# Performance work log

Hardware: AMD Instinct MI355X
Metric: run time of the kernel (lower is better)

The kernel has to match this reference:

```python
import jax, jax.numpy as jnp
import numpy as np

B = 256
H = W = 14
HW = H * W
TS = 0.03  # sigmoid temperature
TC = 0.07  # contrastive temperature
TP_K = int(HW * 0.1)   # 19
TN_K = int(HW * 0.5)   # 98
EPS_NORM = 1e-12
EPS_PD = 1e-6  # torch F.pairwise_distance eps


def _l2norm(x, axis):
    n = jnp.sqrt(jnp.sum(x * x, axis=axis, keepdims=True))
    return x / jnp.maximum(n, EPS_NORM)


def _conv(x, w):
    return jax.lax.conv_general_dilated(
        x, w, window_strides=(1, 1), padding='SAME',
        dimension_numbers=('NCHW', 'OIHW', 'NCHW'))


def setup_inputs() -> dict:
    key = jax.random.key(0)
    ks = jax.random.split(key, 7)
    ev = jax.random.normal(ks[0], (B, 384, H, W), dtype=jnp.float32)
    ea = jax.random.normal(ks[1], (B, 2048), dtype=jnp.float32)
    masks = jax.random.randint(ks[2], (B, H, W), 0, 2).astype(jnp.int32)
    masks = masks.at[:, 0, 0].set(1)  # guarantee nonzero mask area
    W_fc1 = jax.random.normal(ks[3], (512, 2048), dtype=jnp.float32) * 0.02
    W_fc2 = jax.random.normal(ks[4], (512, 512), dtype=jnp.float32) * 0.02
    W_conv1 = jax.random.normal(ks[5], (512, 384, 3, 3), dtype=jnp.float32) * 0.02
    W_conv2 = jax.random.normal(ks[6], (512, 512, 3, 3), dtype=jnp.float32) * 0.02
    return {'ev': ev, 'ea': ea, 'masks': masks, 'W_fc1': W_fc1,
            'W_fc2': W_fc2, 'W_conv1': W_conv1, 'W_conv2': W_conv2}


def reference(ev, ea, masks, W_fc1, W_fc2, W_conv1, W_conv2):
    # Audio_Proj: fc2(relu(fc1(ea)))  -> (B, 512)
    fa = jnp.maximum(ea @ W_fc1.T, 0.0) @ W_fc2.T

    # Visual_Proj: conv2(relu(conv1(ev))) -> (B, 512, 14, 14)
    fv_map = _conv(jnp.maximum(_conv(ev, W_conv1), 0.0), W_conv2)
    fv_map_norm = _l2norm(fv_map, axis=1)

    # masked mean pooling over the Ncut mask -> indicator vector (B, 512)
    m = masks.astype(jnp.float32)
    ind_vec = jnp.sum(fv_map * m[:, None], axis=(2, 3)) / jnp.sum(m, axis=(1, 2))[:, None]
    ind_vec_norm = _l2norm(ind_vec, axis=1)

    # Sij[i, j, p] = <fv_map_norm[i, :, p], ind_vec_norm[j]>  -> (B, B, HW)
    Sij = jnp.einsum('ichw,jc->ijhw', fv_map_norm, ind_vec_norm).reshape(B, B, HW)

    # per-row topk thresholds (kth largest / kth smallest)
    pos_thr = jax.lax.top_k(Sij, TP_K)[0][..., -1:]           # (B, B, 1)
    neg_thr = -jax.lax.top_k(-Sij, TN_K)[0][..., -1:]         # (B, B, 1)

    m_p = jax.nn.sigmoid((Sij - pos_thr) / TS)
    m_n = 1.0 - jax.nn.sigmoid((Sij - neg_thr) / TS)

    SP = jnp.sum(Sij * m_p, axis=-1) / jnp.sum(m_p, axis=-1)  # (B, B)
    SN = jnp.sum(Sij * m_n, axis=-1) / jnp.sum(m_n, axis=-1)  # (B, B)

    logits1 = jnp.concatenate([SP, SN], axis=1) / TC          # (B, 2B)
    logits2 = jnp.concatenate([SP.T, SN.T], axis=1) / TC
    labels = jnp.arange(B)
    loss1 = -jnp.mean(jax.nn.log_softmax(logits1, axis=-1)[labels, labels])
    loss2 = -jnp.mean(jax.nn.log_softmax(logits2, axis=-1)[labels, labels])

    # squared pairwise distance between detached ind_vec and fa (torch eps in diff)
    diff = jax.lax.stop_gradient(ind_vec)[:, None, :] - fa[None, :, :] + EPS_PD
    dist_mat = jnp.sum(diff * diff, axis=-1)                  # (B, B)

    ivn_d = jax.lax.stop_gradient(ind_vec_norm)
    vv_logits = ivn_d @ ivn_d.T
    eye = jnp.eye(B, dtype=jnp.float32)
    w = -vv_logits * (1.0 - eye) + eye
    dist_mat = dist_mat * w

    mask_mat = eye - (1.0 - eye) / (B - 1)
    loss3 = jnp.mean(jnp.maximum(jnp.sum(dist_mat * mask_mat, axis=1) + 0.6, 0.0))
    loss4 = jnp.mean(jnp.maximum(jnp.sum(dist_mat * mask_mat, axis=0) + 0.6, 0.0))

    return ((loss1 + loss2) / 2.0, (loss3 + loss4) / 2.0)
```

## Files before the change

kernel.cpp:

```cpp
#include <hip/hip_runtime.h>
#include <stdint.h>


typedef __attribute__((ext_vector_type(8))) short bf16x8;
typedef __attribute__((ext_vector_type(4))) float f32x4;

__device__ __forceinline__ unsigned short f2bf(float x) {
  unsigned u = __float_as_uint(x);
  unsigned r = u + 0x7FFFu + ((u >> 16) & 1u);
  return (unsigned short)(r >> 16);
}
__device__ __forceinline__ float bf2f(unsigned short h) {
  return __uint_as_float(((unsigned)h) << 16);
}

typedef const __attribute__((address_space(1))) void* gptr1_t;
typedef __attribute__((address_space(3))) void* lptr3_t;
__device__ __forceinline__ void gload_lds16(const void* g, void* l) {
  __builtin_amdgcn_global_load_lds((gptr1_t)g, (lptr3_t)l, 16, 0, 0);
}

__device__ __forceinline__ float waveSum(float v) {
#pragma unroll
  for (int m = 1; m < 64; m <<= 1) v += __shfl_xor(v, m, 64);
  return v;
}
__device__ __forceinline__ float waveMax(float v) {
#pragma unroll
  for (int m = 1; m < 64; m <<= 1) v = fmaxf(v, __shfl_xor(v, m, 64));
  return v;
}
template <int NW>
__device__ __forceinline__ float blockSum(float v) {
  __shared__ float sh[NW];
  v = waveSum(v);
  int wv = threadIdx.x >> 6, ln = threadIdx.x & 63;
  if (ln == 0) sh[wv] = v;
  __syncthreads();
  float r = 0.f;
#pragma unroll
  for (int w = 0; w < NW; ++w) r += sh[w];
  __syncthreads();
  return r;
}
template <int NW>
__device__ __forceinline__ float blockMax(float v) {
  __shared__ float sh[NW];
  v = waveMax(v);
  int wv = threadIdx.x >> 6, ln = threadIdx.x & 63;
  if (ln == 0) sh[wv] = v;
  __syncthreads();
  float r = -3.4e38f;
#pragma unroll
  for (int w = 0; w < NW; ++w) r = fmaxf(r, sh[w]);
  __syncthreads();
  return r;
}

template <int K, int NT, int NTOT, int NLD, bool APAD, bool OPAD, int EPI>
__global__ __launch_bounds__(256, 2) void gemm_k(
    const unsigned short* __restrict__ A, const unsigned short* __restrict__ Bw,
    void* __restrict__ C) {
  __shared__ short As[128 * 64];
  __shared__ short Bs[128 * 64];
  const int tid = threadIdx.x;
  const int wave = tid >> 6, lane = tid & 63;
  const int m0 = blockIdx.x * 128, n0 = blockIdx.y * 128;
  const int rr8 = lane >> 3;
  const int seg = lane & 7;
  const int gseg = seg ^ rr8;
  const int wm = wave >> 1, wn = wave & 1;
  const int quad = lane >> 4, tq = lane & 15;

  int asrc[4], bsrc[4];
#pragma unroll
  for (int i8 = 0; i8 < 4; ++i8) {
    int rloc = wave * 32 + i8 * 8 + rr8;
    int m = m0 + rloc;
    int sr;
    if (APAD) {
      int b = m / 196, p = m - b * 196, h = p / 14, w = p - h * 14;
      sr = b * 256 + (h + 1) * 16 + (w + 1);
    } else
      sr = m;
    asrc[i8] = sr * K + gseg * 8;
    bsrc[i8] = (n0 + rloc) * K + gseg * 8;
  }

  short* As_st[4];
  short* Bs_st[4];
#pragma unroll
  for (int i8 = 0; i8 < 4; ++i8) {
    As_st[i8] = &As[(wave * 32 + i8 * 8) * 64];
    Bs_st[i8] = &Bs[(wave * 32 + i8 * 8) * 64];
  }

  f32x4 acc[4][4];
#pragma unroll
  for (int mi = 0; mi < 4; ++mi)
#pragma unroll
    for (int ni = 0; ni < 4; ++ni) {
      f32x4 z = {0.f, 0.f, 0.f, 0.f};
      acc[mi][ni] = z;
    }

#pragma unroll 1
  for (int t = 0; t < NT; ++t) {
    int adel = 0;
    if (NT > 1) {
      int dh = t / 3 - 1, dw = t - (t / 3) * 3 - 1;
      adel = (dh * 16 + dw) * K;
    }
    const unsigned short* Bt = Bw + (size_t)t * NTOT * K;
#pragma unroll 1
    for (int kc2 = 0; kc2 < K / 64; ++kc2) {
      int kb = kc2 * 64;
      __syncthreads();
#pragma unroll
      for (int i8 = 0; i8 < 4; ++i8)
        gload_lds16(A + asrc[i8] + adel + kb, As_st[i8]);
#pragma unroll
      for (int i8 = 0; i8 < 4; ++i8)
        gload_lds16(Bt + bsrc[i8] + kb, Bs_st[i8]);
      __syncthreads();
#pragma unroll
      for (int h = 0; h < 2; ++h) {
        bf16x8 af[4], bfr[4];
#pragma unroll
        for (int mi = 0; mi < 4; ++mi) {
          int row = wm * 64 + mi * 16 + tq;
          af[mi] = *(const bf16x8*)&As[row * 64 +
                                       (((h << 2) | quad) ^ (row & 7)) * 8];
        }
#pragma unroll
        for (int ni = 0; ni < 4; ++ni) {
          int row = wn * 64 + ni * 16 + tq;
          bfr[ni] = *(const bf16x8*)&Bs[row * 64 +
                                        (((h << 2) | quad) ^ (row & 7)) * 8];
        }
#pragma unroll
        for (int mi = 0; mi < 4; ++mi)
#pragma unroll
          for (int ni = 0; ni < 4; ++ni)
            acc[mi][ni] = __builtin_amdgcn_mfma_f32_16x16x32_bf16(
                af[mi], bfr[ni], acc[mi][ni], 0, 0, 0);
      }
    }
  }

#pragma unroll
  for (int mi = 0; mi < 4; ++mi) {
#pragma unroll
    for (int r = 0; r < 4; ++r) {
      int m = m0 + wm * 64 + mi * 16 + quad * 4 + r;
      int orow;
      if (OPAD) {
        int b = m / 196, p = m - b * 196, h = p / 14, w = p - h * 14;
        orow = b * 256 + (h + 1) * 16 + (w + 1);
      } else
        orow = m;
      size_t obase = (size_t)orow * NLD + n0 + wn * 64 + tq;
#pragma unroll
      for (int ni = 0; ni < 4; ++ni) {
        float v = acc[mi][ni][r];
        size_t idx = obase + ni * 16;
        if (EPI == 0)
          ((unsigned short*)C)[idx] = f2bf(fmaxf(v, 0.f));
        else if (EPI == 1)
          ((unsigned short*)C)[idx] = f2bf(v);
        else
          ((float*)C)[idx] = v;
      }
    }
  }
}


__global__ void prep_cast_k(const float* __restrict__ ea,
                            const float* __restrict__ Wf1,
                            const float* __restrict__ Wf2,
                            unsigned short* __restrict__ eab,
                            unsigned short* __restrict__ wf1b,
                            unsigned short* __restrict__ wf2b) {
  int i = blockIdx.x * 256 + threadIdx.x;
  if (i < 524288)
    eab[i] = f2bf(ea[i]);
  else if (i < 1572864)
    wf1b[i - 524288] = f2bf(Wf1[i - 524288]);
  else
    wf2b[i - 1572864] = f2bf(Wf2[i - 1572864]);
}

template <int CIN>
__global__ void build_wb_k(const float* __restrict__ W,
                           unsigned short* __restrict__ out) {
  int i = blockIdx.x * 256 + threadIdx.x;
  if (i >= 9 * 512 * CIN) return;
  int t = i / (512 * CIN);
  int rem = i - t * (512 * CIN);
  int n = rem / CIN;
  int c = rem - n * CIN;
  out[i] = f2bf(W[(n * CIN + c) * 9 + t]);
}

__global__ void evpad_k(const float* __restrict__ ev,
                        unsigned short* __restrict__ out) {
  int i = blockIdx.x * 256 + threadIdx.x;
  int pr = i / 384, c = i - pr * 384;
  int b = pr >> 8, cell = pr & 255;
  int h = (cell >> 4) - 1, w = (cell & 15) - 1;
  float v = 0.f;
  if ((unsigned)h < 14u && (unsigned)w < 14u)
    v = ev[(b * 384 + c) * 196 + h * 14 + w];
  out[i] = f2bf(v);
}

__global__ void halo_k(unsigned int* __restrict__ x1u) {
  int r = blockIdx.x;
  int b = r / 60, c = r - b * 60;
  int cell;
  if (c < 16) cell = c;
  else if (c < 32) cell = 240 + (c - 16);
  else if (c < 46) cell = (c - 31) * 16;
  else cell = (c - 45) * 16 + 15;
  x1u[(size_t)(b * 256 + cell) * 256 + threadIdx.x] = 0u;
}


__global__ __launch_bounds__(512) void pool_k(
    const unsigned short* __restrict__ fv, const int* __restrict__ masks,
    float* __restrict__ indv) {
  int b = blockIdx.x;
  int w = threadIdx.x >> 6, lane = threadIdx.x & 63;
  __shared__ float red[8][512];
  __shared__ float msh[8];
  float acc[8] = {0.f, 0.f, 0.f, 0.f, 0.f, 0.f, 0.f, 0.f};
  float msum = 0.f;
  for (int p = w; p < 196; p += 8) {
    float m = (float)masks[b * 196 + p];
    msum += m;
    uint4 d = *(const uint4*)(fv + (size_t)(b * 196 + p) * 512 + lane * 8);
    const unsigned short* hp = (const unsigned short*)&d;
#pragma unroll
    for (int k = 0; k < 8; ++k) acc[k] += m * bf2f(hp[k]);
  }
#pragma unroll
  for (int k = 0; k < 8; ++k) red[w][lane * 8 + k] = acc[k];
  if (lane == 0) msh[w] = msum;
  __syncthreads();
  int tid = threadIdx.x;
  float s = 0.f, mtot = 0.f;
#pragma unroll
  for (int ww = 0; ww < 8; ++ww) {
    s += red[ww][tid];
    mtot += msh[ww];
  }
  indv[b * 512 + tid] = s / mtot;
}

__global__ __launch_bounds__(512) void indnorm_k(
    const float* __restrict__ indv, float* __restrict__ indn,
    unsigned short* __restrict__ indnb, unsigned short* __restrict__ ivpb,
    float* __restrict__ Pi) {
  int b = blockIdx.x, tid = threadIdx.x;
  float v = indv[b * 512 + tid];
  float ss = blockSum<8>(v * v);
  float sc = 1.f / fmaxf(sqrtf(ss), 1e-12f);
  float o = v * sc;
  indn[b * 512 + tid] = o;
  indnb[b * 512 + tid] = f2bf(o);
  float ve = v + 1e-6f;
  ivpb[b * 512 + tid] = f2bf(ve);
  float p2 = blockSum<8>(ve * ve);
  if (tid == 0) Pi[b] = p2;
}

__global__ __launch_bounds__(512) void fanorm_k(const float* __restrict__ fa,
                                                unsigned short* __restrict__ fab,
                                                float* __restrict__ Qj) {
  int b = blockIdx.x, tid = threadIdx.x;
  float v = fa[b * 512 + tid];
  fab[b * 512 + tid] = f2bf(v);
  float q = blockSum<8>(v * v);
  if (tid == 0) Qj[b] = q;
}

__global__ __launch_bounds__(256) void rownorm_k(
    const unsigned short* __restrict__ fv, float* __restrict__ rn) {
  int row = blockIdx.x * 4 + (threadIdx.x >> 6);
  int lane = threadIdx.x & 63;
  uint4 d = *(const uint4*)(fv + (size_t)row * 512 + lane * 8);
  const unsigned short* hp = (const unsigned short*)&d;
  float ss = 0.f;
#pragma unroll
  for (int k = 0; k < 8; ++k) {
    float x = bf2f(hp[k]);
    ss += x * x;
  }
  ss = waveSum(ss);
  if (lane == 0) rn[row] = 1.f / fmaxf(sqrtf(ss), 1e-12f);
}


__device__ __forceinline__ float radix_kth(unsigned k0, unsigned k1, unsigned k2,
                                           unsigned k3, int k) {
  unsigned prefix = 0;
  int kk = k;
#pragma unroll 1
  for (int bit = 31; bit >= 8; --bit) {
    unsigned thi = (prefix >> bit) | 1u;
    int c = __popcll(__ballot((k0 >> bit) == thi)) +
            __popcll(__ballot((k1 >> bit) == thi)) +
            __popcll(__ballot((k2 >> bit) == thi)) +
            __popcll(__ballot((k3 >> bit) == thi));
    if (kk <= c)
      prefix |= (1u << bit);
    else
      kk -= c;
  }
  unsigned u = (prefix & 0x80000000u) ? (prefix ^ 0x80000000u) : ~prefix;
  return __uint_as_float(u);
}
__device__ __forceinline__ unsigned sortkey(float x) {
  unsigned u = __float_as_uint(x);
  return u ^ (((int)u >> 31) | 0x80000000u);
}

__global__ __launch_bounds__(256) void spsn_k(const float* __restrict__ Sij,
                                              const float* __restrict__ rn,
                                              float* __restrict__ SP,
                                              float* __restrict__ SN) {
  int i = blockIdx.x, jg = blockIdx.y;
  int tid = threadIdx.x, wave = tid >> 6, lane = tid & 63;
  __shared__ float tile[196 * 65];
#pragma unroll 1
  for (int it = 0; it < 49; ++it) {
    int lin = it * 256 + tid;
    int p = lin >> 6, j = lin & 63;
    tile[p * 65 + j] =
        Sij[(size_t)(i * 196 + p) * 256 + jg * 64 + j] * rn[i * 196 + p];
  }
  __syncthreads();
#pragma unroll 1
  for (int jj = 0; jj < 16; ++jj) {
    int j = jj * 4 + wave;
    float v0 = tile[lane * 65 + j];
    float v1 = tile[(lane + 64) * 65 + j];
    float v2 = tile[(lane + 128) * 65 + j];
    bool val3 = lane < 4;
    float v3 = val3 ? tile[(lane + 192) * 65 + j] : 0.f;
    unsigned k0 = sortkey(v0), k1 = sortkey(v1), k2 = sortkey(v2);
    unsigned k3 = val3 ? sortkey(v3) : 0u;
    float thrP = radix_kth(k0, k1, k2, k3, 19);
    float thrN = radix_kth(k0, k1, k2, k3, 99);
    float spn = 0.f, spd = 0.f, snn = 0.f, snd = 0.f;
    const float invTS = 1.f / 0.03f;
#pragma unroll
    for (int q = 0; q < 4; ++q) {
      float v = (q == 0) ? v0 : (q == 1) ? v1 : (q == 2) ? v2 : v3;
      bool ok = (q < 3) || val3;
      if (ok) {
        float mp = 1.f / (1.f + __expf((thrP - v) * invTS));
        float mn = 1.f / (1.f + __expf((v - thrN) * invTS));
        spn += v * mp;
        spd += mp;
        snn += v * mn;
        snd += mn;
      }
    }
    spn = waveSum(spn); spd = waveSum(spd);
    snn = waveSum(snn); snd = waveSum(snd);
    if (lane == 0) {
      SP[i * 256 + jg * 64 + j] = spn / spd;
      SN[i * 256 + jg * 64 + j] = snn / snd;
    }
  }
}

__global__ __launch_bounds__(256) void loss12_k(const float* __restrict__ SP,
                                                const float* __restrict__ SN,
                                                float* __restrict__ out) {
  int r = blockIdx.x;
  int i = r & 255;
  bool col = r >= 256;
  int tid = threadIdx.x;
  const float invTC = 1.f / 0.07f;
  float a = (col ? SP[tid * 256 + i] : SP[i * 256 + tid]) * invTC;
  float b = (col ? SN[tid * 256 + i] : SN[i * 256 + tid]) * invTC;
  float mx = blockMax<4>(fmaxf(a, b));
  float se = blockSum<4>(__expf(a - mx) + __expf(b - mx));
  float lse = mx + __logf(se);
  if (tid == 0) {
    float diag = SP[i * 256 + i] * invTC;
    atomicAdd(out, -(diag - lse) * (1.f / 512.f));
  }
}

__global__ __launch_bounds__(256) void distcomb_k(
    const float* __restrict__ Pi, const float* __restrict__ Qj,
    const float* __restrict__ X, const float* __restrict__ V,
    float* __restrict__ val, float* __restrict__ out) {
  int i = blockIdx.x, j = threadIdx.x;
  float d = Pi[i] - 2.f * X[i * 256 + j] + Qj[j];
  float w = (i == j) ? 1.f : -V[i * 256 + j];
  float x = d * w;
  val[i * 256 + j] = x;
  __shared__ float diag_sh;
  if (j == i) diag_sh = x;
  float tot = blockSum<4>(x);
  if (j == 0) {
    float rs = diag_sh - (tot - diag_sh) * (1.f / 255.f);
    atomicAdd(out + 1, fmaxf(rs + 0.6f, 0.f) * (1.f / 512.f));
  }
}

__global__ __launch_bounds__(256) void loss4_k(const float* __restrict__ val,
                                               float* __restrict__ out) {
  int j = blockIdx.x, i = threadIdx.x;
  float x = val[i * 256 + j];
  __shared__ float diag_sh;
  if (i == j) diag_sh = x;
  float tot = blockSum<4>(x);
  if (i == 0) {
    float cs = diag_sh - (tot - diag_sh) * (1.f / 255.f);
    atomicAdd(out + 1, fmaxf(cs + 0.6f, 0.f) * (1.f / 512.f));
  }
}


extern "C" void kernel_launch(void* const* d_in, const int* in_sizes, int n_in,
                              void* d_out, int out_size, void* d_ws,
                              size_t ws_size, hipStream_t stream) {
  (void)in_sizes; (void)n_in; (void)out_size; (void)ws_size;
  const float* ev = (const float*)d_in[0];
  const float* ea = (const float*)d_in[1];
  const int* msk = (const int*)d_in[2];
  const float* Wf1 = (const float*)d_in[3];
  const float* Wf2 = (const float*)d_in[4];
  const float* Wc1 = (const float*)d_in[5];
  const float* Wc2 = (const float*)d_in[6];
  float* out = (float*)d_out;
  char* ws = (char*)d_ws;

  size_t off = 0;
  auto alloc = [&](size_t bytes) {
    void* p = ws + off;
    off = (off + bytes + 255) & ~(size_t)255;
    return p;
  };
  unsigned short* evb = (unsigned short*)alloc(51380224);
  unsigned short* fv = evb;
  unsigned short* x1b = (unsigned short*)alloc((size_t)65536 * 512 * 2);
  float* Sij = (float*)x1b;
  unsigned short* wb1 = (unsigned short*)alloc((size_t)9 * 512 * 384 * 2);
  unsigned short* wb2 = (unsigned short*)alloc((size_t)9 * 512 * 512 * 2);
  unsigned short* eab = (unsigned short*)alloc((size_t)256 * 2048 * 2);
  unsigned short* wf1b = (unsigned short*)alloc((size_t)512 * 2048 * 2);
  unsigned short* wf2b = (unsigned short*)alloc((size_t)512 * 512 * 2);
  unsigned short* hb = (unsigned short*)alloc((size_t)256 * 512 * 2);
  float* fa = (float*)alloc((size_t)256 * 512 * 4);
  float* indv = (float*)alloc((size_t)256 * 512 * 4);
  float* indn = (float*)alloc((size_t)256 * 512 * 4);
  unsigned short* indnb = (unsigned short*)alloc((size_t)256 * 512 * 2);
  unsigned short* ivpb = (unsigned short*)alloc((size_t)256 * 512 * 2);
  unsigned short* fab = (unsigned short*)alloc((size_t)256 * 512 * 2);
  float* Pi = (float*)alloc(256 * 4);
  float* Qj = (float*)alloc(256 * 4);
  float* Xm = (float*)alloc((size_t)256 * 256 * 4);
  float* Vm = (float*)alloc((size_t)256 * 256 * 4);
  float* rn = (float*)alloc((size_t)50176 * 4);
  float* SP = (float*)alloc((size_t)256 * 256 * 4);
  float* SN = (float*)alloc((size_t)256 * 256 * 4);
  float* val = (float*)alloc((size_t)256 * 256 * 4);

  hipMemsetAsync(out, 0, 2 * sizeof(float), stream);

  prep_cast_k<<<7168, 256, 0, stream>>>(ea, Wf1, Wf2, eab, wf1b, wf2b);
  build_wb_k<384><<<(9 * 512 * 384) / 256, 256, 0, stream>>>(Wc1, wb1);
  build_wb_k<512><<<(9 * 512 * 512) / 256, 256, 0, stream>>>(Wc2, wb2);
  evpad_k<<<(65536 * 384) / 256, 256, 0, stream>>>(ev, evb);
  halo_k<<<15360, 256, 0, stream>>>((unsigned int*)x1b);

  gemm_k<384, 9, 512, 512, true, true, 0>
      <<<dim3(392, 4), 256, 0, stream>>>(evb, wb1, x1b);
  gemm_k<2048, 1, 512, 512, false, false, 0>
      <<<dim3(2, 4), 256, 0, stream>>>(eab, wf1b, hb);
  gemm_k<512, 1, 512, 512, false, false, 2>
      <<<dim3(2, 4), 256, 0, stream>>>(hb, wf2b, fa);
  gemm_k<512, 9, 512, 512, true, false, 1>
      <<<dim3(392, 4), 256, 0, stream>>>(x1b, wb2, fv);

  pool_k<<<256, 512, 0, stream>>>(fv, msk, indv);
  fanorm_k<<<256, 512, 0, stream>>>(fa, fab, Qj);
  indnorm_k<<<256, 512, 0, stream>>>(indv, indn, indnb, ivpb, Pi);
  rownorm_k<<<12544, 256, 0, stream>>>(fv, rn);

  gemm_k<512, 1, 256, 256, false, false, 2>
      <<<dim3(392, 2), 256, 0, stream>>>(fv, indnb, Sij);
  gemm_k<512, 1, 256, 256, false, false, 2>
      <<<dim3(2, 2), 256, 0, stream>>>(ivpb, fab, Xm);
  gemm_k<512, 1, 256, 256, false, false, 2>
      <<<dim3(2, 2), 256, 0, stream>>>(indnb, indnb, Vm);

  spsn_k<<<dim3(256, 4), 256, 0, stream>>>(Sij, rn, SP, SN);
  loss12_k<<<512, 256, 0, stream>>>(SP, SN, out);
  distcomb_k<<<256, 256, 0, stream>>>(Pi, Qj, Xm, Vm, val, out);
  loss4_k<<<256, 256, 0, stream>>>(val, out);
}
```

Baseline: 923.9 us.

## Reuse haloed activation tile across all nine conv taps with double-buffered weights

Replaces the per-tap implicit-GEMM conv loop with a kernel that loads a 256-row haloed window of padded activations once per K-chunk and reuses it for all nine taps, indexing shifted rows in LDS. Weight tiles for the next tap are prefetched into a second LDS buffer while the current tap computes. Activation global/L2 traffic per conv drops by about nine times, at the cost of more LDS and more barriers per chunk. Also coalesces the ev padding transpose through shared memory and folds the row-norm computation into the pooling kernel, removing a separate pass over fv.

After: 972.1 us. 1.05x slower.

```diff
diff --git a/kernel.cpp b/kernel.cpp
--- a/kernel.cpp
+++ b/kernel.cpp
@@ -57,8 +57,120 @@
   return r;
 }
 
-template <int K, int NT, int NTOT, int NLD, bool APAD, bool OPAD, int EPI>
-__global__ __launch_bounds__(256, 2) void gemm_k(
+__device__ __forceinline__ int padrow(int m) {
+  int b = m / 196, p = m - b * 196, h = p / 14, w = p - h * 14;
+  return b * 256 + (h + 1) * 16 + (w + 1);
+}
+
+template <int K, int EPI>
+__global__ __launch_bounds__(512, 4) void convtap_k(
+    const unsigned short* __restrict__ A, const unsigned short* __restrict__ Bw,
+    unsigned short* __restrict__ C) {
+  __shared__ short Ah[256 * 64];
+  __shared__ short Bb[2][128 * 64];
+  const int tid = threadIdx.x;
+  const int wave = tid >> 6, lane = tid & 63;
+  const int wm = wave >> 2, wn = wave & 3;
+  const int quad = lane >> 4, tq = lane & 15;
+  const int rr8 = lane >> 3, seg = lane & 7, gseg = seg ^ rr8;
+  const int m0 = blockIdx.x * 128, n0 = blockIdx.y * 128;
+  const int base = padrow(m0) - 17;
+
+  int prow[4];
+#pragma unroll
+  for (int mi = 0; mi < 4; ++mi)
+    prow[mi] = padrow(m0 + wm * 64 + mi * 16 + tq) - base;
+
+  size_t asrc[4];
+#pragma unroll
+  for (int i = 0; i < 4; ++i) {
+    int r = base + i * 64 + wave * 8 + rr8;
+    if (r > 65535) r = 65535;
+    asrc[i] = (size_t)r * K + gseg * 8;
+  }
+  size_t bsrc[2];
+#pragma unroll
+  for (int i = 0; i < 2; ++i)
+    bsrc[i] = (size_t)(n0 + i * 64 + wave * 8 + rr8) * K + gseg * 8;
+  const size_t btap = (size_t)512 * K;
+
+  f32x4 acc[4][2];
+#pragma unroll
+  for (int mi = 0; mi < 4; ++mi)
+#pragma unroll
+    for (int ni = 0; ni < 2; ++ni) {
+      f32x4 z = {0.f, 0.f, 0.f, 0.f};
+      acc[mi][ni] = z;
+    }
+
+#pragma unroll 1
+  for (int kc = 0; kc < K / 64; ++kc) {
+    const int kb = kc * 64;
+    __syncthreads();
+#pragma unroll
+    for (int i = 0; i < 4; ++i)
+      gload_lds16(A + asrc[i] + kb, &Ah[(i * 64 + wave * 8) * 64]);
+#pragma unroll
+    for (int i = 0; i < 2; ++i)
+      gload_lds16(Bw + bsrc[i] + kb, &Bb[0][(i * 64 + wave * 8) * 64]);
+    __syncthreads();
+#pragma unroll 1
+    for (int t = 0; t < 9; ++t) {
+      if (t < 8) {
+        const unsigned short* Bt1 = Bw + (size_t)(t + 1) * btap;
+#pragma unroll
+        for (int i = 0; i < 2; ++i)
+          gload_lds16(Bt1 + bsrc[i] + kb,
+                      &Bb[(t + 1) & 1][(i * 64 + wave * 8) * 64]);
+      }
+      int t3 = t / 3;
+      int delta = (t3 - 1) * 16 + (t - t3 * 3 - 1);
+      const short* Bcur = Bb[t & 1];
+#pragma unroll
+      for (int h = 0; h < 2; ++h) {
+        bf16x8 af[4], bfr[2];
+#pragma unroll
+        for (int mi = 0; mi < 4; ++mi) {
+          int r = prow[mi] + delta;
+          af[mi] = *(const bf16x8*)&Ah[r * 64 +
+                                       ((((h << 2) | quad) ^ (r & 7)) << 3)];
+        }
+#pragma unroll
+        for (int ni = 0; ni < 2; ++ni) {
+          int r = wn * 32 + ni * 16 + tq;
+          bfr[ni] = *(const bf16x8*)&Bcur[r * 64 +
+                                          ((((h << 2) | quad) ^ (r & 7)) << 3)];
+        }
+#pragma unroll
+        for (int mi = 0; mi < 4; ++mi)
+#pragma unroll
+          for (int ni = 0; ni < 2; ++ni)
+            acc[mi][ni] = __builtin_amdgcn_mfma_f32_16x16x32_bf16(
+                af[mi], bfr[ni], acc[mi][ni], 0, 0, 0);
+      }
+      if (t < 8) __syncthreads();
+    }
+  }
+
+#pragma unroll
+  for (int mi = 0; mi < 4; ++mi) {
+#pragma unroll
+    for (int r = 0; r < 4; ++r) {
+      int m = m0 + wm * 64 + mi * 16 + quad * 4 + r;
+      int orow = (EPI == 0) ? padrow(m) : m;
+      size_t ob = (size_t)orow * 512 + n0 + wn * 32 + tq;
+#pragma unroll
+      for (int ni = 0; ni < 2; ++ni) {
+        float v = acc[mi][ni][r];
+        if (EPI == 0) v = fmaxf(v, 0.f);
+        C[ob + ni * 16] = f2bf(v);
+      }
+    }
+  }
+}
+
+template <int K, int NLD, int EPI>
+__global__ __launch_bounds__(256, 2) void gemm1_k(
     const unsigned short* __restrict__ A, const unsigned short* __restrict__ Bw,
     void* __restrict__ C) {
   __shared__ short As[128 * 64];
@@ -66,33 +178,16 @@
   const int tid = threadIdx.x;
   const int wave = tid >> 6, lane = tid & 63;
   const int m0 = blockIdx.x * 128, n0 = blockIdx.y * 128;
-  const int rr8 = lane >> 3;
-  const int seg = lane & 7;
-  const int gseg = seg ^ rr8;
+  const int rr8 = lane >> 3, seg = lane & 7, gseg = seg ^ rr8;
   const int wm = wave >> 1, wn = wave & 1;
   const int quad = lane >> 4, tq = lane & 15;
 
-  int asrc[4], bsrc[4];
+  size_t asrc[4], bsrc[4];
 #pragma unroll
   for (int i8 = 0; i8 < 4; ++i8) {
     int rloc = wave * 32 + i8 * 8 + rr8;
-    int m = m0 + rloc;
-    int sr;
-    if (APAD) {
-      int b = m / 196, p = m - b * 196, h = p / 14, w = p - h * 14;
-      sr = b * 256 + (h + 1) * 16 + (w + 1);
-    } else
-      sr = m;
-    asrc[i8] = sr * K + gseg * 8;
-    bsrc[i8] = (n0 + rloc) * K + gseg * 8;
-  }
-
-  short* As_st[4];
-  short* Bs_st[4];
-#pragma unroll
-  for (int i8 = 0; i8 < 4; ++i8) {
-    As_st[i8] = &As[(wave * 32 + i8 * 8) * 64];
-    Bs_st[i8] = &Bs[(wave * 32 + i8 * 8) * 64];
+    asrc[i8] = (size_t)(m0 + rloc) * K + gseg * 8;
+    bsrc[i8] = (size_t)(n0 + rloc) * K + gseg * 8;
   }
 
   f32x4 acc[4][4];
@@ -105,46 +200,36 @@
     }
 
 #pragma unroll 1
-  for (int t = 0; t < NT; ++t) {
-    int adel = 0;
-    if (NT > 1) {
-      int dh = t / 3 - 1, dw = t - (t / 3) * 3 - 1;
-      adel = (dh * 16 + dw) * K;
-    }
-    const unsigned short* Bt = Bw + (size_t)t * NTOT * K;
-#pragma unroll 1
-    for (int kc2 = 0; kc2 < K / 64; ++kc2) {
-      int kb = kc2 * 64;
-      __syncthreads();
-#pragma unroll
-      for (int i8 = 0; i8 < 4; ++i8)
-        gload_lds16(A + asrc[i8] + adel + kb, As_st[i8]);
-#pragma unroll
-      for (int i8 = 0; i8 < 4; ++i8)
-        gload_lds16(Bt + bsrc[i8] + kb, Bs_st[i8]);
-      __syncthreads();
-#pragma unroll
-      for (int h = 0; h < 2; ++h) {
-        bf16x8 af[4], bfr[4];
-#pragma unroll
-        for (int mi = 0; mi < 4; ++mi) {
-          int row = wm * 64 + mi * 16 + tq;
-          af[mi] = *(const bf16x8*)&As[row * 64 +
-                                       (((h << 2) | quad) ^ (row & 7)) * 8];
-        }
-#pragma unroll
-        for (int ni = 0; ni < 4; ++ni) {
-          int row = wn * 64 + ni * 16 + tq;
-          bfr[ni] = *(const bf16x8*)&Bs[row * 64 +
-                                        (((h << 2) | quad) ^ (row & 7)) * 8];
-        }
-#pragma unroll
-        for (int mi = 0; mi < 4; ++mi)
-#pragma unroll
-          for (int ni = 0; ni < 4; ++ni)
-            acc[mi][ni] = __builtin_amdgcn_mfma_f32_16x16x32_bf16(
-                af[mi], bfr[ni], acc[mi][ni], 0, 0, 0);
-      }
+  for (int kc2 = 0; kc2 < K / 64; ++kc2) {
+    int kb = kc2 * 64;
+    __syncthreads();
+#pragma unroll
+    for (int i8 = 0; i8 < 4; ++i8) {
+      gload_lds16(A + asrc[i8] + kb, &As[(wave * 32 + i8 * 8) * 64]);
+      gload_lds16(Bw + bsrc[i8] + kb, &Bs[(wave * 32 + i8 * 8) * 64]);
+    }
+    __syncthreads();
+#pragma unroll
+    for (int h = 0; h < 2; ++h) {
+      bf16x8 af[4], bfr[4];
+#pragma unroll
+      for (int mi = 0; mi < 4; ++mi) {
+        int row = wm * 64 + mi * 16 + tq;
+        af[mi] = *(const bf16x8*)&As[row * 64 +
+                                     ((((h << 2) | quad) ^ (row & 7)) << 3)];
+      }
+#pragma unroll
+      for (int ni = 0; ni < 4; ++ni) {
+        int row = wn * 64 + ni * 16 + tq;
+        bfr[ni] = *(const bf16x8*)&Bs[row * 64 +
+                                      ((((h << 2) | quad) ^ (row & 7)) << 3)];
+      }
+#pragma unroll
+      for (int mi = 0; mi < 4; ++mi)
+#pragma unroll
+        for (int ni = 0; ni < 4; ++ni)
+          acc[mi][ni] = __builtin_amdgcn_mfma_f32_16x16x32_bf16(
+              af[mi], bfr[ni], acc[mi][ni], 0, 0, 0);
     }
   }
 
@@ -153,21 +238,13 @@
 #pragma unroll
     for (int r = 0; r < 4; ++r) {
       int m = m0 + wm * 64 + mi * 16 + quad * 4 + r;
-      int orow;
-      if (OPAD) {
-        int b = m / 196, p = m - b * 196, h = p / 14, w = p - h * 14;
-        orow = b * 256 + (h + 1) * 16 + (w + 1);
-      } else
-        orow = m;
-      size_t obase = (size_t)orow * NLD + n0 + wn * 64 + tq;
+      size_t obase = (size_t)m * NLD + n0 + wn * 64 + tq;
 #pragma unroll
       for (int ni = 0; ni < 4; ++ni) {
         float v = acc[mi][ni][r];
         size_t idx = obase + ni * 16;
         if (EPI == 0)
           ((unsigned short*)C)[idx] = f2bf(fmaxf(v, 0.f));
-        else if (EPI == 1)
-          ((unsigned short*)C)[idx] = f2bf(v);
         else
           ((float*)C)[idx] = v;
       }
@@ -203,16 +280,29 @@
   out[i] = f2bf(W[(n * CIN + c) * 9 + t]);
 }
 
-__global__ void evpad_k(const float* __restrict__ ev,
-                        unsigned short* __restrict__ out) {
-  int i = blockIdx.x * 256 + threadIdx.x;
-  int pr = i / 384, c = i - pr * 384;
-  int b = pr >> 8, cell = pr & 255;
-  int h = (cell >> 4) - 1, w = (cell & 15) - 1;
-  float v = 0.f;
-  if ((unsigned)h < 14u && (unsigned)w < 14u)
-    v = ev[(b * 384 + c) * 196 + h * 14 + w];
-  out[i] = f2bf(v);
+__global__ __launch_bounds__(256) void evpad_k(const float* __restrict__ ev,
+                                               unsigned short* __restrict__ out) {
+  int b = blockIdx.x, ct = blockIdx.y;
+  __shared__ float tile[64][197];
+  int tid = threadIdx.x;
+  const float* src = ev + ((size_t)b * 384 + ct * 64) * 196;
+#pragma unroll 1
+  for (int it = 0; it < 49; ++it) {
+    int idx = it * 256 + tid;
+    int c = idx / 196, p = idx - c * 196;
+    tile[c][p] = src[idx];
+  }
+  __syncthreads();
+  unsigned short* dst = out + (size_t)b * 256 * 384 + ct * 64;
+#pragma unroll 1
+  for (int it = 0; it < 64; ++it) {
+    int idx = it * 256 + tid;
+    int cell = idx >> 6, c = idx & 63;
+    int h = (cell >> 4) - 1, w = (cell & 15) - 1;
+    float v = ((unsigned)h < 14u && (unsigned)w < 14u) ? tile[c][h * 14 + w]
+                                                       : 0.f;
+    dst[(size_t)cell * 384 + c] = f2bf(v);
+  }
 }
 
 __global__ void halo_k(unsigned int* __restrict__ x1u) {
@@ -229,7 +319,7 @@
 
 __global__ __launch_bounds__(512) void pool_k(
     const unsigned short* __restrict__ fv, const int* __restrict__ masks,
-    float* __restrict__ indv) {
+    float* __restrict__ indv, float* __restrict__ rn) {
   int b = blockIdx.x;
   int w = threadIdx.x >> 6, lane = threadIdx.x & 63;
   __shared__ float red[8][512];
@@ -241,8 +331,15 @@
     msum += m;
     uint4 d = *(const uint4*)(fv + (size_t)(b * 196 + p) * 512 + lane * 8);
     const unsigned short* hp = (const unsigned short*)&d;
-#pragma unroll
-    for (int k = 0; k < 8; ++k) acc[k] += m * bf2f(hp[k]);
+    float ss = 0.f;
+#pragma unroll
+    for (int k = 0; k < 8; ++k) {
+      float x = bf2f(hp[k]);
+      ss += x * x;
+      acc[k] += m * x;
+    }
+    ss = waveSum(ss);
+    if (lane == 0) rn[b * 196 + p] = 1.f / fmaxf(sqrtf(ss), 1e-12f);
   }
 #pragma unroll
   for (int k = 0; k < 8; ++k) red[w][lane * 8 + k] = acc[k];
@@ -283,22 +380,6 @@
   fab[b * 512 + tid] = f2bf(v);
   float q = blockSum<8>(v * v);
   if (tid == 0) Qj[b] = q;
-}
-
-__global__ __launch_bounds__(256) void rownorm_k(
-    const unsigned short* __restrict__ fv, float* __restrict__ rn) {
-  int row = blockIdx.x * 4 + (threadIdx.x >> 6);
-  int lane = threadIdx.x & 63;
-  uint4 d = *(const uint4*)(fv + (size_t)row * 512 + lane * 8);
-  const unsigned short* hp = (const unsigned short*)&d;
-  float ss = 0.f;
-#pragma unroll
-  for (int k = 0; k < 8; ++k) {
-    float x = bf2f(hp[k]);
-    ss += x * x;
-  }
-  ss = waveSum(ss);
-  if (lane == 0) rn[row] = 1.f / fmaxf(sqrtf(ss), 1e-12f);
 }
 
 
@@ -448,7 +529,7 @@
     off = (off + bytes + 255) & ~(size_t)255;
     return p;
   };
-  unsigned short* evb = (unsigned short*)alloc(51380224);
+  unsigned short* evb = (unsigned short*)alloc((size_t)50176 * 512 * 2);
   unsigned short* fv = evb;
   unsigned short* x1b = (unsigned short*)alloc((size_t)65536 * 512 * 2);
   float* Sij = (float*)x1b;
@@ -478,29 +559,21 @@
   prep_cast_k<<<7168, 256, 0, stream>>>(ea, Wf1, Wf2, eab, wf1b, wf2b);
   build_wb_k<384><<<(9 * 512 * 384) / 256, 256, 0, stream>>>(Wc1, wb1);
   build_wb_k<512><<<(9 * 512 * 512) / 256, 256, 0, stream>>>(Wc2, wb2);
-  evpad_k<<<(65536 * 384) / 256, 256, 0, stream>>>(ev, evb);
+  evpad_k<<<dim3(256, 6), 256, 0, stream>>>(ev, evb);
   halo_k<<<15360, 256, 0, stream>>>((unsigned int*)x1b);
 
-  gemm_k<384, 9, 512, 512, true, true, 0>
-      <<<dim3(392, 4), 256, 0, stream>>>(evb, wb1, x1b);
-  gemm_k<2048, 1, 512, 512, false, false, 0>
-      <<<dim3(2, 4), 256, 0, stream>>>(eab, wf1b, hb);
-  gemm_k<512, 1, 512, 512, false, false, 2>
-      <<<dim3(2, 4), 256, 0, stream>>>(hb, wf2b, fa);
-  gemm_k<512, 9, 512, 512, true, false, 1>
-      <<<dim3(392, 4), 256, 0, stream>>>(x1b, wb2, fv);
-
-  pool_k<<<256, 512, 0, stream>>>(fv, msk, indv);
+  convtap_k<384, 0><<<dim3(392, 4), 512, 0, stream>>>(evb, wb1, x1b);
+  gemm1_k<2048, 512, 0><<<dim3(2, 4), 256, 0, stream>>>(eab, wf1b, hb);
+  gemm1_k<512, 512, 2><<<dim3(2, 4), 256, 0, stream>>>(hb, wf2b, fa);
+  convtap_k<512, 1><<<dim3(392, 4), 512, 0, stream>>>(x1b, wb2, fv);
+
+  pool_k<<<256, 512, 0, stream>>>(fv, msk, indv, rn);
   fanorm_k<<<256, 512, 0, stream>>>(fa, fab, Qj);
   indnorm_k<<<256, 512, 0, stream>>>(indv, indn, indnb, ivpb, Pi);
-  rownorm_k<<<12544, 256, 0, stream>>>(fv, rn);
-
-  gemm_k<512, 1, 256, 256, false, false, 2>
-      <<<dim3(392, 2), 256, 0, stream>>>(fv, indnb, Sij);
-  gemm_k<512, 1, 256, 256, false, false, 2>
-      <<<dim3(2, 2), 256, 0, stream>>>(ivpb, fab, Xm);
-  gemm_k<512, 1, 256, 256, false, false, 2>
-      <<<dim3(2, 2), 256, 0, stream>>>(indnb, indnb, Vm);
+
+  gemm1_k<512, 256, 2><<<dim3(392, 2), 256, 0, stream>>>(fv, indnb, Sij);
+  gemm1_k<512, 256, 2><<<dim3(2, 2), 256, 0, stream>>>(ivpb, fab, Xm);
+  gemm1_k<512, 256, 2><<<dim3(2, 2), 256, 0, stream>>>(indnb, indnb, Vm);
 
   spsn_k<<<dim3(256, 4), 256, 0, stream>>>(Sij, rn, SP, SN);
   loss12_k<<<512, 256, 0, stream>>>(SP, SN, out);
```
